# Kernel optimization log

Hardware: AMD Instinct MI355X
Metric: run time of the kernel (lower is better)

## Reference

```python
import jax, jax.numpy as jnp
import numpy as np

B, S, D, H = 4, 1024, 2048, 16
DH = D // H  # 128
THETA = 10000.0


def setup_inputs() -> dict:
    key = jax.random.key(0)
    k1, k2, k3 = jax.random.split(key, 3)
    std_qkv = np.sqrt(2.0 / (D + 3 * D)).astype(np.float32)
    std_out = np.sqrt(2.0 / (D + D)).astype(np.float32)
    x = jax.random.normal(k1, (B, S, D), jnp.float32)
    w_qkv = jax.random.normal(k2, (D, 3 * D), jnp.float32) * std_qkv
    w_out = jax.random.normal(k3, (D, D), jnp.float32) * std_out
    # matrix-based RoPE table: [max_seq, d_head//2, 2, 2]
    freqs = jnp.arange(S, dtype=jnp.float32)[:, None] / THETA ** (
        2.0 * jnp.arange(DH // 2, dtype=jnp.float32) / DH)[None, :]
    eye = jnp.array([[1.0, 0.0], [0.0, 1.0]], jnp.float32)
    rot = jnp.array([[0.0, -1.0], [1.0, 0.0]], jnp.float32)
    rope_matrix = (jnp.cos(freqs)[:, :, None, None] * eye
                   + jnp.sin(freqs)[:, :, None, None] * rot)
    token_positions = jnp.arange(S, dtype=jnp.int32)
    return {"x": x, "w_qkv": w_qkv, "w_out": w_out,
            "rope_matrix": rope_matrix, "token_positions": token_positions}


def _apply_rope(t, pe):
    # t: [B, H, S, DH]; pe: [S, DH//2, 2, 2] (gathered by token_positions)
    tr = t.reshape(*t.shape[:-1], DH // 2, 2)  # interleaved (even, odd) pairs
    out = jnp.einsum('bhski,skoi->bhsko', tr, pe)
    return out.reshape(t.shape)


def reference(x, w_qkv, w_out, rope_matrix, token_positions):
    qkv = jnp.einsum('bsd,df->bsf', x, w_qkv)          # [B,S,3D]
    q, k, v = jnp.split(qkv, 3, axis=-1)
    to_heads = lambda t: t.reshape(B, S, H, DH).transpose(0, 2, 1, 3)
    q, k, v = to_heads(q), to_heads(k), to_heads(v)    # [B,H,S,DH]
    pe = rope_matrix[token_positions]                  # [S, DH//2, 2, 2]
    q = _apply_rope(q, pe)
    k = _apply_rope(k, pe)
    scores = jnp.einsum('bhqd,bhkd->bhqk', q, k) / np.float32(np.sqrt(DH))
    causal = jnp.tril(jnp.ones((S, S), dtype=bool))
    scores = jnp.where(causal, scores, -jnp.inf)
    attn = jax.nn.softmax(scores, axis=-1)
    ctx = jnp.einsum('bhqk,bhkd->bhqd', attn, v)       # [B,H,S,DH]
    ctx = ctx.transpose(0, 2, 1, 3).reshape(B, S, D)
    return jnp.einsum('bsd,df->bsf', ctx, w_out)
```

## Files before the change

kernel.cpp:

```cpp
#include <hip/hip_runtime.h>
#include <hip/hip_bf16.h>
#include <math.h>

#define Bn 4
#define Sn 1024
#define Dn 2048
#define Hn 16
#define DHn 128
#define BS (Bn * Sn)
#define QKVC (3 * Dn)

typedef __attribute__((ext_vector_type(8))) short short8;
typedef __attribute__((ext_vector_type(4))) float float4v;

__device__ inline unsigned short f2bf(float x) {
  union { float f; unsigned int u; } v; v.f = x;
  unsigned int r = v.u + 0x7fffu + ((v.u >> 16) & 1u);
  return (unsigned short)(r >> 16);
}
__device__ inline float bf2f(unsigned short b) {
  union { unsigned int u; float f; } v; v.u = ((unsigned int)b) << 16;
  return v.f;
}

__device__ __forceinline__ void gload16(const unsigned short* g, unsigned short* l) {
  __builtin_amdgcn_global_load_lds(
      (const __attribute__((address_space(1))) unsigned int*)g,
      (__attribute__((address_space(3))) unsigned int*)l, 16, 0, 0);
}

__device__ void tc_body(const float* __restrict__ w, unsigned short* __restrict__ wT,
                        int K, int N, int bx, int by, int tid,
                        unsigned short (*t)[72]) {
  const int c0 = bx * 64;
  const int r0 = by * 64;
  const int r = tid >> 2;
  const int cb = (tid & 3) * 16;
#pragma unroll
  for (int it = 0; it < 4; ++it) {
    float4 v = *reinterpret_cast<const float4*>(&w[(long)(r0 + r) * N + c0 + cb + 4 * it]);
    t[r][cb + 4 * it + 0] = f2bf(v.x);
    t[r][cb + 4 * it + 1] = f2bf(v.y);
    t[r][cb + 4 * it + 2] = f2bf(v.z);
    t[r][cb + 4 * it + 3] = f2bf(v.w);
  }
  __syncthreads();
  unsigned short o[16];
#pragma unroll
  for (int e = 0; e < 16; ++e) o[e] = t[cb + e][r];
  unsigned short* dst = &wT[(long)(c0 + r) * K + r0 + cb];
  *reinterpret_cast<short8*>(dst) = *reinterpret_cast<short8*>(&o[0]);
  *reinterpret_cast<short8*>(dst + 8) = *reinterpret_cast<short8*>(&o[8]);
}

__global__ __launch_bounds__(256) void prep_all(
    const float* __restrict__ x, const float* __restrict__ w_qkv,
    const float* __restrict__ w_out, unsigned short* __restrict__ x16,
    unsigned short* __restrict__ wqkvT, unsigned short* __restrict__ woutT) {
  __shared__ unsigned short t[64][72];
  const int bid = blockIdx.x;
  const int tid = threadIdx.x;
  if (bid < 4096) {
    const int id = bid * 256 + tid;
    const float4* p = reinterpret_cast<const float4*>(x) + 2 * (size_t)id;
    float4 a = p[0], b = p[1];
    short8 o;
    o[0] = (short)f2bf(a.x); o[1] = (short)f2bf(a.y);
    o[2] = (short)f2bf(a.z); o[3] = (short)f2bf(a.w);
    o[4] = (short)f2bf(b.x); o[5] = (short)f2bf(b.y);
    o[6] = (short)f2bf(b.z); o[7] = (short)f2bf(b.w);
    *reinterpret_cast<short8*>(x16 + 8 * (size_t)id) = o;
  } else if (bid < 7168) {
    const int lb = bid - 4096;
    tc_body(w_qkv, wqkvT, Dn, QKVC, lb % 96, lb / 96, tid, t);
  } else {
    const int lb = bid - 7168;
    tc_body(w_out, woutT, Dn, Dn, lb % 32, lb / 32, tid, t);
  }
}

#define ABUF(buf) ((buf) * 8192)
#define BBUF(buf) (16384 + (buf) * 8192)

#define TILE_MAP()                                                             \
  const int nwg = gridDim.x * gridDim.y;                                       \
  const int bid = blockIdx.y * gridDim.x + blockIdx.x;                         \
  const int swz = (bid & 7) * (nwg >> 3) + (bid >> 3);                         \
  const int t_ = swz & 255, grp_ = swz >> 8;                                   \
  const int m0 = (t_ >> 3) * 128;                                              \
  const int n0 = ((t_ & 7) + grp_ * 8) * 128;

#define GEMM128_LOOP(A_, BT_, K_)                                              \
  STAGE(A_ + (long)m0 * K_, ABUF(0));                                          \
  STAGE(BT_ + (long)n0 * K_, BBUF(0));                                         \
  __syncthreads();                                                             \
  for (int t = 0; t < nt; ++t) {                                               \
    const int cb = t & 1;                                                      \
    if (t + 1 < nt) {                                                          \
      const long To = (long)(t + 1) * 64;                                      \
      STAGE(A_ + (long)m0 * K_ + To, ABUF(cb ^ 1));                            \
      STAGE(BT_ + (long)n0 * K_ + To, BBUF(cb ^ 1));                           \
    }                                                                          \
    short8 afr[4][2], bfr[4][2];                                               \
    _Pragma("unroll") for (int mi = 0; mi < 4; ++mi)                           \
      _Pragma("unroll") for (int ks = 0; ks < 2; ++ks)                         \
        afr[mi][ks] = *(const short8*)(lds + ABUF(cb) +                        \
            (wr * 64 + mi * 16 + c) * 64 + (((ks * 4 + g) ^ cg7) << 3));       \
    _Pragma("unroll") for (int ni = 0; ni < 4; ++ni)                           \
      _Pragma("unroll") for (int ks = 0; ks < 2; ++ks)                         \
        bfr[ni][ks] = *(const short8*)(lds + BBUF(cb) +                        \
            (wc * 64 + ni * 16 + c) * 64 + (((ks * 4 + g) ^ cg7) << 3));       \
    __builtin_amdgcn_s_setprio(1);                                             \
    _Pragma("unroll") for (int mi = 0; mi < 4; ++mi)                           \
      _Pragma("unroll") for (int ni = 0; ni < 4; ++ni)                         \
        _Pragma("unroll") for (int ks = 0; ks < 2; ++ks)                       \
          acc[mi][ni] = __builtin_amdgcn_mfma_f32_16x16x32_bf16(               \
              afr[mi][ks], bfr[ni][ks], acc[mi][ni], 0, 0, 0);                 \
    __builtin_amdgcn_s_setprio(0);                                             \
    __syncthreads();                                                           \
  }

__global__ __launch_bounds__(256, 2) void gemm_qkv(
    const unsigned short* __restrict__ A, const unsigned short* __restrict__ BT,
    const float* __restrict__ rope, const int* __restrict__ tpos,
    unsigned short* __restrict__ qR, unsigned short* __restrict__ kR,
    unsigned short* __restrict__ vT, int K) {
  __shared__ unsigned short lds[32768];
  const int tid = threadIdx.x;
  const int wid = tid >> 6, lane = tid & 63;
  const int c = lane & 15, g = lane >> 4;
  const int wr = wid >> 1, wc = wid & 1;
  const int cg7 = c & 7;

  TILE_MAP()

  const int nt = K >> 6;

  float4v acc[4][4];
#pragma unroll
  for (int i = 0; i < 4; ++i)
#pragma unroll
    for (int j = 0; j < 4; ++j) acc[i][j] = (float4v){0.f, 0.f, 0.f, 0.f};

  auto STAGE = [&](const unsigned short* gbase, int sbase) {
#pragma unroll
    for (int j = 0; j < 4; ++j) {
      const int ch = j * 256 + tid;
      const int r = ch >> 3;
      const int wo = (ch & 7) ^ (r & 7);
      gload16(gbase + (long)r * K + wo * 8, lds + sbase + j * 2048 + wid * 512);
    }
  };

  GEMM128_LOOP(A, BT, K)

  const int type = n0 >> 11;
  const int h = (n0 & 2047) >> 7;
  const long bh = (long)((m0 >> 10) * Hn + h);
  const int s0 = m0 & 1023;

  if (type == 2) {
#pragma unroll
    for (int mi = 0; mi < 4; ++mi)
#pragma unroll
      for (int ni = 0; ni < 4; ++ni)
#pragma unroll
        for (int j = 0; j < 4; ++j) {
          const int mm = wr * 64 + mi * 16 + g * 4 + j;
          const int nn = wc * 64 + ni * 16 + c;
          lds[nn * 136 + mm] = f2bf(acc[mi][ni][j]);
        }
    __syncthreads();
    unsigned short* dst = vT + bh * (long)DHn * Sn + s0;
#pragma unroll
    for (int it = 0; it < 8; ++it) {
      const int cid = it * 256 + tid;
      const int d = cid >> 4;
      const int sl = (cid & 15) * 8;
      short8 v = *reinterpret_cast<const short8*>(lds + d * 136 + sl);
      *reinterpret_cast<short8*>(dst + (long)d * Sn + sl) = v;
    }
  } else {
#pragma unroll
    for (int mi = 0; mi < 4; ++mi)
#pragma unroll
      for (int ni = 0; ni < 4; ++ni)
#pragma unroll
        for (int j = 0; j < 4; ++j) {
          const int mm = wr * 64 + mi * 16 + g * 4 + j;
          const int nn = wc * 64 + ni * 16 + c;
          lds[mm * 136 + nn] = f2bf(acc[mi][ni][j]);
        }
    __syncthreads();
    unsigned short* dst = (type == 0 ? qR : kR) + (bh * Sn + s0) * DHn;
    const float qsc = (type == 0) ? 0.1275174213f : 1.0f;
#pragma unroll
    for (int it = 0; it < 8; ++it) {
      const int cid = it * 256 + tid;
      const int r = cid >> 4;
      const int colc = (cid & 15) * 8;
      union { short8 v; unsigned short u[8]; } iw, ow;
      iw.v = *reinterpret_cast<const short8*>(lds + r * 136 + colc);
      const int pos = tpos[s0 + r];
      const float4* pe = reinterpret_cast<const float4*>(rope) +
                         (long)pos * 64 + (colc >> 1);
#pragma unroll
      for (int p = 0; p < 4; ++p) {
        const float4 m2 = pe[p];
        const float xx = bf2f(iw.u[2 * p]), yy = bf2f(iw.u[2 * p + 1]);
        ow.u[2 * p]     = f2bf((m2.x * xx + m2.y * yy) * qsc);
        ow.u[2 * p + 1] = f2bf((m2.z * xx + m2.w * yy) * qsc);
      }
      *reinterpret_cast<short8*>(dst + (long)r * DHn + colc) = ow.v;
    }
  }
}

__global__ __launch_bounds__(256, 2) void gemm_out(
    const unsigned short* __restrict__ A, const unsigned short* __restrict__ BT,
    float* __restrict__ Cout, int N, int K) {
  __shared__ unsigned short lds[32768];
  const int tid = threadIdx.x;
  const int wid = tid >> 6, lane = tid & 63;
  const int c = lane & 15, g = lane >> 4;
  const int wr = wid >> 1, wc = wid & 1;
  const int cg7 = c & 7;

  TILE_MAP()

  const int nt = K >> 6;

  float4v acc[4][4];
#pragma unroll
  for (int i = 0; i < 4; ++i)
#pragma unroll
    for (int j = 0; j < 4; ++j) acc[i][j] = (float4v){0.f, 0.f, 0.f, 0.f};

  auto STAGE = [&](const unsigned short* gbase, int sbase) {
#pragma unroll
    for (int j = 0; j < 4; ++j) {
      const int ch = j * 256 + tid;
      const int r = ch >> 3;
      const int wo = (ch & 7) ^ (r & 7);
      gload16(gbase + (long)r * K + wo * 8, lds + sbase + j * 2048 + wid * 512);
    }
  };

  GEMM128_LOOP(A, BT, K)

#pragma unroll
  for (int mi = 0; mi < 4; ++mi)
#pragma unroll
    for (int ni = 0; ni < 4; ++ni)
#pragma unroll
      for (int j = 0; j < 4; ++j) {
        const int m = m0 + wr * 64 + mi * 16 + g * 4 + j;
        const int n = n0 + wc * 64 + ni * 16 + c;
        Cout[(long)m * N + n] = acc[mi][ni][j];
      }
}
#undef GEMM128_LOOP
#undef TILE_MAP

__global__ __launch_bounds__(256, 2) void attn_mfma(
    const unsigned short* __restrict__ qR, const unsigned short* __restrict__ kR,
    const unsigned short* __restrict__ vTd, unsigned short* __restrict__ ctx) {
  __shared__ unsigned short lds[32768];
  __shared__ unsigned short Ps[4][16][72];
  const int n = blockIdx.x;
  const int qp = (n < 256) ? (7 - (n >> 6)) : ((n - 256) >> 6);
  const int hb = n & 63;
  const int h = hb >> 2, b = hb & 3;
  const int tid = threadIdx.x, wid = tid >> 6, lane = tid & 63;
  const int c = lane & 15, g = lane >> 4, cg7 = c & 7;
  const long bh = (long)(b * Hn + h);
  const unsigned short* kbase = kR + bh * Sn * DHn;
  const unsigned short* vbase = vTd + bh * DHn * Sn;

  short8 qf[2][4];
#pragma unroll
  for (int sub = 0; sub < 2; ++sub) {
    const unsigned short* qrow =
        qR + (bh * Sn + qp * 128 + sub * 64 + wid * 16 + c) * DHn;
#pragma unroll
    for (int kc = 0; kc < 4; ++kc)
      qf[sub][kc] = *reinterpret_cast<const short8*>(qrow + kc * 32 + g * 8);
  }

  auto STAGE = [&](int kt, int buf) {
#pragma unroll
    for (int j = 0; j < 4; ++j) {
      const int ch = j * 256 + tid;
      const int r = ch >> 4, wd = ch & 15;
      const int ws = (wd & 8) | ((wd & 7) ^ (r & 7));
      gload16(kbase + (long)kt * 8192 + r * 128 + ws * 8,
              lds + buf * 8192 + j * 2048 + wid * 512);
    }
#pragma unroll
    for (int j = 0; j < 4; ++j) {
      const int ch = j * 256 + tid;
      const int d = ch >> 3, sw = ch & 7;
      gload16(vbase + (long)d * Sn + kt * 64 + ((sw ^ (d & 7)) << 3),
              lds + 16384 + buf * 8192 + j * 2048 + wid * 512);
    }
  };

  float m[2] = {-INFINITY, -INFINITY}, lsum[2] = {0.f, 0.f};
  float4v otA[8], otB[8];
#pragma unroll
  for (int fd = 0; fd < 8; ++fd) {
    otA[fd] = (float4v){0.f, 0.f, 0.f, 0.f};
    otB[fd] = (float4v){0.f, 0.f, 0.f, 0.f};
  }

  const int ntt = 2 * qp + 2;
  STAGE(0, 0);
  __syncthreads();
  int cur = 0;

  for (int kt = 0; kt < ntt; ++kt) {
    if (kt + 1 < ntt) STAGE(kt + 1, cur ^ 1);

#pragma unroll
    for (int sub = 0; sub < 2; ++sub) {
      if (sub == 0 && kt == ntt - 1) continue;
      float4v* ot = (sub == 0) ? otA : otB;

      float4v scv[4];
#pragma unroll
      for (int f = 0; f < 4; ++f) scv[f] = (float4v){0.f, 0.f, 0.f, 0.f};
      __builtin_amdgcn_s_setprio(1);
#pragma unroll
      for (int f = 0; f < 4; ++f)
#pragma unroll
        for (int kc = 0; kc < 4; ++kc) {
          const int wp = kc * 4 + g;
          const int ws = (wp & 8) | ((wp & 7) ^ cg7);
          short8 kf = *reinterpret_cast<const short8*>(
              lds + cur * 8192 + (f * 16 + c) * 128 + ws * 8);
          scv[f] = __builtin_amdgcn_mfma_f32_16x16x32_bf16(kf, qf[sub][kc],
                                                           scv[f], 0, 0, 0);
        }
      __builtin_amdgcn_s_setprio(0);

      if (kt == 2 * qp + sub) {
        const int qloc = wid * 16 + c;
#pragma unroll
        for (int f = 0; f < 4; ++f)
#pragma unroll
          for (int j = 0; j < 4; ++j)
            if (f * 16 + g * 4 + j > qloc) scv[f][j] = -INFINITY;
      }

      float tmax = -INFINITY;
#pragma unroll
      for (int f = 0; f < 4; ++f)
#pragma unroll
        for (int j = 0; j < 4; ++j) tmax = fmaxf(tmax, scv[f][j]);
      tmax = fmaxf(tmax, __shfl_xor(tmax, 16));
      tmax = fmaxf(tmax, __shfl_xor(tmax, 32));

      float mnew, corr;
      if (__all(tmax <= m[sub] + 8.f)) {
        mnew = m[sub]; corr = 1.f;
      } else {
        mnew = fmaxf(m[sub], tmax);
        corr = exp2f(m[sub] - mnew);
#pragma unroll
        for (int fd = 0; fd < 8; ++fd) ot[fd] *= corr;
      }
      float psum = 0.f;
#pragma unroll
      for (int f = 0; f < 4; ++f)
#pragma unroll
        for (int j = 0; j < 4; ++j) {
          scv[f][j] = exp2f(scv[f][j] - mnew);
          psum += scv[f][j];
        }
      psum += __shfl_xor(psum, 16);
      psum += __shfl_xor(psum, 32);
      lsum[sub] = lsum[sub] * corr + psum;
      m[sub] = mnew;

#pragma unroll
      for (int f = 0; f < 4; ++f) {
        unsigned int lo = (unsigned)f2bf(scv[f][0]) | ((unsigned)f2bf(scv[f][1]) << 16);
        unsigned int hi = (unsigned)f2bf(scv[f][2]) | ((unsigned)f2bf(scv[f][3]) << 16);
        uint2 pk; pk.x = lo; pk.y = hi;
        *reinterpret_cast<uint2*>(&Ps[wid][c][f * 16 + g * 4]) = pk;
      }

      short8 pf0 = *reinterpret_cast<const short8*>(&Ps[wid][c][g * 8]);
      short8 pf1 = *reinterpret_cast<const short8*>(&Ps[wid][c][32 + g * 8]);
      __builtin_amdgcn_s_setprio(1);
#pragma unroll
      for (int fd = 0; fd < 8; ++fd) {
        short8 vf0 = *reinterpret_cast<const short8*>(
            lds + 16384 + cur * 8192 + (fd * 16 + c) * 64 + ((g ^ cg7) << 3));
        short8 vf1 = *reinterpret_cast<const short8*>(
            lds + 16384 + cur * 8192 + (fd * 16 + c) * 64 + (((g + 4) ^ cg7) << 3));
        ot[fd] = __builtin_amdgcn_mfma_f32_16x16x32_bf16(vf0, pf0, ot[fd], 0, 0, 0);
        ot[fd] = __builtin_amdgcn_mfma_f32_16x16x32_bf16(vf1, pf1, ot[fd], 0, 0, 0);
      }
      __builtin_amdgcn_s_setprio(0);
    }

    __syncthreads();
    cur ^= 1;
  }

#pragma unroll
  for (int sub = 0; sub < 2; ++sub) {
    const float4v* ot = (sub == 0) ? otA : otB;
    const float inv = 1.0f / lsum[sub];
    unsigned short* orow =
        ctx + (long)(b * Sn + qp * 128 + sub * 64 + wid * 16 + c) * Dn + h * DHn;
#pragma unroll
    for (int fd = 0; fd < 8; ++fd) {
      const int d = fd * 16 + g * 4;
      uint2 pk;
      pk.x = (unsigned)f2bf(ot[fd][0] * inv) | ((unsigned)f2bf(ot[fd][1] * inv) << 16);
      pk.y = (unsigned)f2bf(ot[fd][2] * inv) | ((unsigned)f2bf(ot[fd][3] * inv) << 16);
      *reinterpret_cast<uint2*>(orow + d) = pk;
    }
  }
}

extern "C" void kernel_launch(void* const* d_in, const int* in_sizes, int n_in,
                              void* d_out, int out_size, void* d_ws, size_t ws_size,
                              hipStream_t stream) {
  const float* x     = (const float*)d_in[0];
  const float* w_qkv = (const float*)d_in[1];
  const float* w_out = (const float*)d_in[2];
  const float* rope  = (const float*)d_in[3];
  const int*   tpos  = (const int*)d_in[4];
  float* out = (float*)d_out;

  unsigned short* x16    = (unsigned short*)d_ws;
  unsigned short* wqkvT  = x16 + (size_t)BS * Dn;
  unsigned short* woutT  = wqkvT + (size_t)Dn * QKVC;
  unsigned short* qR     = woutT + (size_t)Dn * Dn;
  unsigned short* kR     = qR + (size_t)BS * Dn;
  unsigned short* vT16   = kR + (size_t)BS * Dn;
  unsigned short* ctx16  = vT16 + (size_t)BS * Dn;

  prep_all<<<8192, 256, 0, stream>>>(x, w_qkv, w_out, x16, wqkvT, woutT);
  {
    dim3 grid(BS / 128, QKVC / 128);
    gemm_qkv<<<grid, 256, 0, stream>>>(x16, wqkvT, rope, tpos, qR, kR, vT16, Dn);
  }
  attn_mfma<<<512, 256, 0, stream>>>(qR, kR, vT16, ctx16);
  {
    dim3 grid(BS / 128, Dn / 128);
    gemm_out<<<grid, 256, 0, stream>>>(ctx16, woutT, out, Dn, Dn);
  }
}
```

Before: 210.0 us.

## Halve GEMM K-tile to 32 to shrink LDS and raise occupancy

Both projection GEMMs now stage a 32-wide K slice per iteration instead of 64, which halves the double-buffered LDS footprint to 32 KB and changes the XOR swizzle to match the narrower rows. Launch bounds are raised from 2 to 5 blocks per CU to exploit the smaller LDS and hide latency with more resident waves. The QKV epilogue is split into two halves that reuse the smaller LDS buffer with a 72-element stride, adding extra barriers. The cost is twice as many loop iterations and barriers per tile, and tighter register limits under the higher launch bound.

Result: slower. 712.4 us (+239.2%).

```diff
diff --git a/kernel.cpp b/kernel.cpp
--- a/kernel.cpp
+++ b/kernel.cpp
@@ -79,8 +79,8 @@
   }
 }
 
-#define ABUF(buf) ((buf) * 8192)
-#define BBUF(buf) (16384 + (buf) * 8192)
+#define ABUF(buf) ((buf) * 4096)
+#define BBUF(buf) (8192 + (buf) * 4096)
 
 #define TILE_MAP()                                                             \
   const int nwg = gridDim.x * gridDim.y;                                       \
@@ -90,51 +90,48 @@
   const int m0 = (t_ >> 3) * 128;                                              \
   const int n0 = ((t_ & 7) + grp_ * 8) * 128;
 
-#define GEMM128_LOOP(A_, BT_, K_)                                              \
+#define GEMM32_LOOP(A_, BT_, K_)                                               \
   STAGE(A_ + (long)m0 * K_, ABUF(0));                                          \
   STAGE(BT_ + (long)n0 * K_, BBUF(0));                                         \
   __syncthreads();                                                             \
   for (int t = 0; t < nt; ++t) {                                               \
     const int cb = t & 1;                                                      \
     if (t + 1 < nt) {                                                          \
-      const long To = (long)(t + 1) * 64;                                      \
+      const long To = (long)(t + 1) * 32;                                      \
       STAGE(A_ + (long)m0 * K_ + To, ABUF(cb ^ 1));                            \
       STAGE(BT_ + (long)n0 * K_ + To, BBUF(cb ^ 1));                           \
     }                                                                          \
-    short8 afr[4][2], bfr[4][2];                                               \
+    short8 afr[4], bfr[4];                                                     \
     _Pragma("unroll") for (int mi = 0; mi < 4; ++mi)                           \
-      _Pragma("unroll") for (int ks = 0; ks < 2; ++ks)                         \
-        afr[mi][ks] = *(const short8*)(lds + ABUF(cb) +                        \
-            (wr * 64 + mi * 16 + c) * 64 + (((ks * 4 + g) ^ cg7) << 3));       \
+      afr[mi] = *(const short8*)(lds + ABUF(cb) +                              \
+          (wr * 64 + mi * 16 + c) * 32 + ((g ^ cg2) << 3));                    \
     _Pragma("unroll") for (int ni = 0; ni < 4; ++ni)                           \
-      _Pragma("unroll") for (int ks = 0; ks < 2; ++ks)                         \
-        bfr[ni][ks] = *(const short8*)(lds + BBUF(cb) +                        \
-            (wc * 64 + ni * 16 + c) * 64 + (((ks * 4 + g) ^ cg7) << 3));       \
+      bfr[ni] = *(const short8*)(lds + BBUF(cb) +                              \
+          (wc * 64 + ni * 16 + c) * 32 + ((g ^ cg2) << 3));                    \
     __builtin_amdgcn_s_setprio(1);                                             \
     _Pragma("unroll") for (int mi = 0; mi < 4; ++mi)                           \
       _Pragma("unroll") for (int ni = 0; ni < 4; ++ni)                         \
-        _Pragma("unroll") for (int ks = 0; ks < 2; ++ks)                       \
-          acc[mi][ni] = __builtin_amdgcn_mfma_f32_16x16x32_bf16(               \
-              afr[mi][ks], bfr[ni][ks], acc[mi][ni], 0, 0, 0);                 \
+        acc[mi][ni] = __builtin_amdgcn_mfma_f32_16x16x32_bf16(                 \
+            afr[mi], bfr[ni], acc[mi][ni], 0, 0, 0);                           \
     __builtin_amdgcn_s_setprio(0);                                             \
     __syncthreads();                                                           \
   }
 
-__global__ __launch_bounds__(256, 2) void gemm_qkv(
+__global__ __launch_bounds__(256, 5) void gemm_qkv(
     const unsigned short* __restrict__ A, const unsigned short* __restrict__ BT,
     const float* __restrict__ rope, const int* __restrict__ tpos,
     unsigned short* __restrict__ qR, unsigned short* __restrict__ kR,
     unsigned short* __restrict__ vT, int K) {
-  __shared__ unsigned short lds[32768];
+  __shared__ unsigned short lds[16384];
   const int tid = threadIdx.x;
   const int wid = tid >> 6, lane = tid & 63;
   const int c = lane & 15, g = lane >> 4;
   const int wr = wid >> 1, wc = wid & 1;
-  const int cg7 = c & 7;
+  const int cg2 = (c >> 1) & 3;
 
   TILE_MAP()
 
-  const int nt = K >> 6;
+  const int nt = K >> 5;
 
   float4v acc[4][4];
 #pragma unroll
@@ -144,15 +141,15 @@
 
   auto STAGE = [&](const unsigned short* gbase, int sbase) {
 #pragma unroll
-    for (int j = 0; j < 4; ++j) {
+    for (int j = 0; j < 2; ++j) {
       const int ch = j * 256 + tid;
-      const int r = ch >> 3;
-      const int wo = (ch & 7) ^ (r & 7);
+      const int r = ch >> 2;
+      const int wo = (ch & 3) ^ ((r >> 1) & 3);
       gload16(gbase + (long)r * K + wo * 8, lds + sbase + j * 2048 + wid * 512);
     }
   };
 
-  GEMM128_LOOP(A, BT, K)
+  GEMM32_LOOP(A, BT, K)
 
   const int type = n0 >> 11;
   const int h = (n0 & 2047) >> 7;
@@ -161,74 +158,87 @@
 
   if (type == 2) {
 #pragma unroll
-    for (int mi = 0; mi < 4; ++mi)
-#pragma unroll
-      for (int ni = 0; ni < 4; ++ni)
-#pragma unroll
-        for (int j = 0; j < 4; ++j) {
-          const int mm = wr * 64 + mi * 16 + g * 4 + j;
-          const int nn = wc * 64 + ni * 16 + c;
-          lds[nn * 136 + mm] = f2bf(acc[mi][ni][j]);
+    for (int half = 0; half < 2; ++half) {
+      if (wr == half) {
+#pragma unroll
+        for (int mi = 0; mi < 4; ++mi)
+#pragma unroll
+          for (int ni = 0; ni < 4; ++ni)
+#pragma unroll
+            for (int j = 0; j < 4; ++j) {
+              const int mml = mi * 16 + g * 4 + j;
+              const int nn = wc * 64 + ni * 16 + c;
+              lds[nn * 72 + mml] = f2bf(acc[mi][ni][j]);
+            }
+      }
+      __syncthreads();
+      unsigned short* dst = vT + bh * (long)DHn * Sn + s0 + half * 64;
+#pragma unroll
+      for (int it = 0; it < 4; ++it) {
+        const int cid = it * 256 + tid;
+        const int d = cid >> 3;
+        const int sl = (cid & 7) * 8;
+        short8 v = *reinterpret_cast<const short8*>(lds + d * 72 + sl);
+        *reinterpret_cast<short8*>(dst + (long)d * Sn + sl) = v;
+      }
+      __syncthreads();
+    }
+  } else {
+    unsigned short* base = (type == 0 ? qR : kR) + (bh * Sn + s0) * DHn;
+    const float qsc = (type == 0) ? 0.1275174213f : 1.0f;
+#pragma unroll
+    for (int half = 0; half < 2; ++half) {
+      if (wc == half) {
+#pragma unroll
+        for (int mi = 0; mi < 4; ++mi)
+#pragma unroll
+          for (int ni = 0; ni < 4; ++ni)
+#pragma unroll
+            for (int j = 0; j < 4; ++j) {
+              const int mm = wr * 64 + mi * 16 + g * 4 + j;
+              const int nnl = ni * 16 + c;
+              lds[mm * 72 + nnl] = f2bf(acc[mi][ni][j]);
+            }
+      }
+      __syncthreads();
+#pragma unroll
+      for (int it = 0; it < 4; ++it) {
+        const int cid = it * 256 + tid;
+        const int r = cid >> 3;
+        const int colc = (cid & 7) * 8;
+        const int gcol = half * 64 + colc;
+        union { short8 v; unsigned short u[8]; } iw, ow;
+        iw.v = *reinterpret_cast<const short8*>(lds + r * 72 + colc);
+        const int pos = tpos[s0 + r];
+        const float4* pe = reinterpret_cast<const float4*>(rope) +
+                           (long)pos * 64 + (gcol >> 1);
+#pragma unroll
+        for (int p = 0; p < 4; ++p) {
+          const float4 m2 = pe[p];
+          const float xx = bf2f(iw.u[2 * p]), yy = bf2f(iw.u[2 * p + 1]);
+          ow.u[2 * p]     = f2bf((m2.x * xx + m2.y * yy) * qsc);
+          ow.u[2 * p + 1] = f2bf((m2.z * xx + m2.w * yy) * qsc);
         }
-    __syncthreads();
-    unsigned short* dst = vT + bh * (long)DHn * Sn + s0;
-#pragma unroll
-    for (int it = 0; it < 8; ++it) {
-      const int cid = it * 256 + tid;
-      const int d = cid >> 4;
-      const int sl = (cid & 15) * 8;
-      short8 v = *reinterpret_cast<const short8*>(lds + d * 136 + sl);
-      *reinterpret_cast<short8*>(dst + (long)d * Sn + sl) = v;
-    }
-  } else {
-#pragma unroll
-    for (int mi = 0; mi < 4; ++mi)
-#pragma unroll
-      for (int ni = 0; ni < 4; ++ni)
-#pragma unroll
-        for (int j = 0; j < 4; ++j) {
-          const int mm = wr * 64 + mi * 16 + g * 4 + j;
-          const int nn = wc * 64 + ni * 16 + c;
-          lds[mm * 136 + nn] = f2bf(acc[mi][ni][j]);
-        }
-    __syncthreads();
-    unsigned short* dst = (type == 0 ? qR : kR) + (bh * Sn + s0) * DHn;
-    const float qsc = (type == 0) ? 0.1275174213f : 1.0f;
-#pragma unroll
-    for (int it = 0; it < 8; ++it) {
-      const int cid = it * 256 + tid;
-      const int r = cid >> 4;
-      const int colc = (cid & 15) * 8;
-      union { short8 v; unsigned short u[8]; } iw, ow;
-      iw.v = *reinterpret_cast<const short8*>(lds + r * 136 + colc);
-      const int pos = tpos[s0 + r];
-      const float4* pe = reinterpret_cast<const float4*>(rope) +
-                         (long)pos * 64 + (colc >> 1);
-#pragma unroll
-      for (int p = 0; p < 4; ++p) {
-        const float4 m2 = pe[p];
-        const float xx = bf2f(iw.u[2 * p]), yy = bf2f(iw.u[2 * p + 1]);
-        ow.u[2 * p]     = f2bf((m2.x * xx + m2.y * yy) * qsc);
-        ow.u[2 * p + 1] = f2bf((m2.z * xx + m2.w * yy) * qsc);
-      }
-      *reinterpret_cast<short8*>(dst + (long)r * DHn + colc) = ow.v;
-    }
-  }
-}
-
-__global__ __launch_bounds__(256, 2) void gemm_out(
+        *reinterpret_cast<short8*>(base + (long)r * DHn + gcol) = ow.v;
+      }
+      __syncthreads();
+    }
+  }
+}
+
+__global__ __launch_bounds__(256, 5) void gemm_out(
     const unsigned short* __restrict__ A, const unsigned short* __restrict__ BT,
     float* __restrict__ Cout, int N, int K) {
-  __shared__ unsigned short lds[32768];
+  __shared__ unsigned short lds[16384];
   const int tid = threadIdx.x;
   const int wid = tid >> 6, lane = tid & 63;
   const int c = lane & 15, g = lane >> 4;
   const int wr = wid >> 1, wc = wid & 1;
-  const int cg7 = c & 7;
+  const int cg2 = (c >> 1) & 3;
 
   TILE_MAP()
 
-  const int nt = K >> 6;
+  const int nt = K >> 5;
 
   float4v acc[4][4];
 #pragma unroll
@@ -238,15 +248,15 @@
 
   auto STAGE = [&](const unsigned short* gbase, int sbase) {
 #pragma unroll
-    for (int j = 0; j < 4; ++j) {
+    for (int j = 0; j < 2; ++j) {
       const int ch = j * 256 + tid;
-      const int r = ch >> 3;
-      const int wo = (ch & 7) ^ (r & 7);
+      const int r = ch >> 2;
+      const int wo = (ch & 3) ^ ((r >> 1) & 3);
       gload16(gbase + (long)r * K + wo * 8, lds + sbase + j * 2048 + wid * 512);
     }
   };
 
-  GEMM128_LOOP(A, BT, K)
+  GEMM32_LOOP(A, BT, K)
 
 #pragma unroll
   for (int mi = 0; mi < 4; ++mi)
@@ -259,7 +269,7 @@
         Cout[(long)m * N + n] = acc[mi][ni][j];
       }
 }
-#undef GEMM128_LOOP
+#undef GEMM32_LOOP
 #undef TILE_MAP
 
 __global__ __launch_bounds__(256, 2) void attn_mfma(
```
